# Optimization experiments

Hardware: AMD Instinct MI355X
Metric: run time of the kernel (lower is better)

## Reference

```python
import jax, jax.numpy as jnp
import numpy as np

N_NODES = 50000
N_EDGES = 800000
N_FEATS = 64
K_HOPS = 3


def setup_inputs() -> dict:
    key = jax.random.key(0)
    k1, k2, k3 = jax.random.split(key, 3)
    x = jax.random.normal(k1, (N_NODES, N_FEATS), dtype=jnp.float32)
    edge_index = jax.random.randint(k2, (2, N_EDGES), 0, N_NODES, dtype=jnp.int32)
    # SGConv linear: out_channels = 1 (hardcoded in Net)
    W = jax.random.normal(k3, (1, N_FEATS), dtype=jnp.float32) / np.sqrt(N_FEATS)
    b = jnp.zeros((1,), dtype=jnp.float32)
    return {"x": x, "edge_index": edge_index, "W": W, "b": b}


def reference(x, edge_index, W, b):
    # SGConv: X' = (D^-1/2 (A + I) D^-1/2)^K X @ W.T + b
    N = x.shape[0]
    self_loops = jnp.arange(N, dtype=edge_index.dtype)
    row = jnp.concatenate([edge_index[0], self_loops])  # source nodes (x_j)
    col = jnp.concatenate([edge_index[1], self_loops])  # destination nodes
    # gcn_norm: degree computed at destination with unit edge weights
    deg = jax.ops.segment_sum(jnp.ones(row.shape[0], x.dtype), col, num_segments=N)
    dinv = jnp.where(deg > 0, jax.lax.rsqrt(deg), jnp.zeros_like(deg))
    norm = dinv[row] * dinv[col]  # [E + N]
    # K hops of normalized sparse propagation: out[col] += norm * x[row]
    for _ in range(K_HOPS):
        x = jax.ops.segment_sum(norm[:, None] * x[row], col, num_segments=N)
    return x @ W.T + b  # [N, 1]
```

## Files before the change

kernel.cpp:

```cpp
#include <hip/hip_runtime.h>
#include <hip/hip_bf16.h>

#define N_NODES 50000
#define N_EDGES 800000
#define N_FEATS 64
#define EB4     (N_EDGES / 4)
#define NBUCK   256
#define BRANGE  196
#define CAPB    4096
#define BZT     1024
#define HOPT    1024


__global__ void __launch_bounds__(BZT) k_bucketize(
    const int* __restrict__ row, const int* __restrict__ col,
    int* __restrict__ gcur, unsigned* __restrict__ recs)
{
    __shared__ int s_cnt[NBUCK];
    __shared__ int s_base[NBUCK];
    const int t = threadIdx.x;
    if (t < NBUCK) s_cnt[t] = 0;
    __syncthreads();

    const int g = blockIdx.x * BZT + t;
    const bool valid = g < EB4;
    int4 c4, r4;
    int bk[4], rk[4];
    if (valid) {
        c4 = ((const int4*)col)[g];
        r4 = ((const int4*)row)[g];
        bk[0] = c4.x / BRANGE; rk[0] = atomicAdd(&s_cnt[bk[0]], 1);
        bk[1] = c4.y / BRANGE; rk[1] = atomicAdd(&s_cnt[bk[1]], 1);
        bk[2] = c4.z / BRANGE; rk[2] = atomicAdd(&s_cnt[bk[2]], 1);
        bk[3] = c4.w / BRANGE; rk[3] = atomicAdd(&s_cnt[bk[3]], 1);
    }
    __syncthreads();
    if (t < NBUCK) {
        int n = s_cnt[t];
        s_base[t] = n ? atomicAdd(&gcur[t], n) : 0;
    }
    __syncthreads();
    if (valid) {
        int cc[4] = {c4.x, c4.y, c4.z, c4.w};
        int rr[4] = {r4.x, r4.y, r4.z, r4.w};
        #pragma unroll
        for (int i = 0; i < 4; i++) {
            int slot = s_base[bk[i]] + rk[i];
            unsigned rec = ((unsigned)(cc[i] - bk[i] * BRANGE) << 16) | (unsigned)rr[i];
            if (slot < CAPB) recs[(size_t)bk[i] * CAPB + slot] = rec;
        }
    }
}

__global__ void __launch_bounds__(512) k_prep(
    const int* __restrict__ gcur, const unsigned* __restrict__ recs,
    const float* __restrict__ x, const float* __restrict__ w,
    float* __restrict__ dinv, float* __restrict__ z0)
{
    __shared__ int   s_cnt[BRANGE];
    __shared__ float s_dinv[BRANGE];
    const int t = threadIdx.x;
    const int blk = blockIdx.x;
    const int own0 = blk * BRANGE;
    if (t < BRANGE) s_cnt[t] = 0;
    __syncthreads();

    const int sz  = min(gcur[blk], CAPB);
    const int sz2 = sz >> 1;
    const uint2* rb2 = (const uint2*)(recs + (size_t)blk * CAPB);
    for (int e = t; e < sz2; e += 512) {
        uint2 r = rb2[e];
        atomicAdd(&s_cnt[r.x >> 16], 1);
        atomicAdd(&s_cnt[r.y >> 16], 1);
    }
    if (t == 0 && (sz & 1)) {
        unsigned r = recs[(size_t)blk * CAPB + sz - 1];
        atomicAdd(&s_cnt[r >> 16], 1);
    }
    __syncthreads();

    if (t < BRANGE) {
        float d = rsqrtf((float)(s_cnt[t] + 1));
        s_dinv[t] = d;
        int node = own0 + t;
        if (node < N_NODES) dinv[node] = d;
    }
    __syncthreads();

    if (t < BRANGE) {
        int node = own0 + t;
        if (node < N_NODES) {
            const float4* xr = (const float4*)(x + (size_t)node * N_FEATS);
            const float4* wr = (const float4*)w;
            float acc = 0.0f;
            #pragma unroll
            for (int k = 0; k < N_FEATS / 4; k++) {
                float4 v = xr[k];
                float4 u = wr[k];
                acc += v.x * u.x + v.y * u.y + v.z * u.z + v.w * u.w;
            }
            z0[node] = s_dinv[t] * acc;
        }
    }
}

template <bool FINAL>
__global__ void __launch_bounds__(HOPT) k_hop(
    const int* __restrict__ gcur, const unsigned* __restrict__ recs,
    const float* __restrict__ dinv, const float* __restrict__ zin,
    float* __restrict__ out, const float* __restrict__ bptr)
{
    __shared__ float acc[BRANGE];
    const int t = threadIdx.x;
    const int blk = blockIdx.x;
    if (t < BRANGE) acc[t] = 0.0f;
    __syncthreads();
    const int sz  = min(gcur[blk], CAPB);
    const int sz2 = sz >> 1;
    const uint2* rb2 = (const uint2*)(recs + (size_t)blk * CAPB);
    for (int e = t; e < sz2; e += HOPT) {
        uint2 r = rb2[e];
        atomicAdd(&acc[r.x >> 16], zin[r.x & 0xFFFFu]);
        atomicAdd(&acc[r.y >> 16], zin[r.y & 0xFFFFu]);
    }
    if (t == 0 && (sz & 1)) {
        unsigned r = recs[(size_t)blk * CAPB + sz - 1];
        atomicAdd(&acc[r >> 16], zin[r & 0xFFFFu]);
    }
    __syncthreads();
    if (t < BRANGE) {
        int node = blk * BRANGE + t;
        if (node < N_NODES) {
            float d = dinv[node];
            float v = zin[node] + acc[t];
            out[node] = FINAL ? (d * v + bptr[0]) : (d * d * v);
        }
    }
}


extern "C" void kernel_launch(void* const* d_in, const int* in_sizes, int n_in,
                              void* d_out, int out_size, void* d_ws, size_t ws_size,
                              hipStream_t stream) {
    const float* x  = (const float*)d_in[0];
    const int*   ei = (const int*)d_in[1];
    const float* W  = (const float*)d_in[2];
    const float* b  = (const float*)d_in[3];
    float* out = (float*)d_out;

    const int* row = ei;
    const int* col = ei + N_EDGES;

    int*      gcur = (int*)d_ws;
    unsigned* recs = (unsigned*)(gcur + NBUCK);
    float*    dinv = (float*)(recs + (size_t)NBUCK * CAPB);
    float*    z0   = dinv + N_NODES;
    float*    z1   = z0 + N_NODES;

    hipMemsetAsync(gcur, 0, NBUCK * sizeof(int), stream);

    k_bucketize<<<(EB4 + BZT - 1) / BZT, BZT, 0, stream>>>(row, col, gcur, recs);
    k_prep<<<NBUCK, 512, 0, stream>>>(gcur, recs, x, W, dinv, z0);

    k_hop<false><<<NBUCK, HOPT, 0, stream>>>(gcur, recs, dinv, z0, z1, nullptr);
    k_hop<false><<<NBUCK, HOPT, 0, stream>>>(gcur, recs, dinv, z1, z0, nullptr);
    k_hop<true ><<<NBUCK, HOPT, 0, stream>>>(gcur, recs, dinv, z0, out, b);
}
```

Measured before the change: 102.0 us.

## Stage bucketized edge records in LDS for coalesced writes; widen prep and hop loads

The bucketize kernel now computes a block-local prefix sum over bucket counts and stages records in shared memory sorted by bucket, then writes them out contiguously, so global stores to each bucket become coalesced rather than scattered. The prep kernel moves to 1024 threads and splits each node's 64-feature dot product across 4 lanes, reduced with shuffles. The hop kernel reads four records per uint4 load and issues all four gathers before the LDS atomics. The trade-off is 32KB of extra shared memory per bucketize block, which may limit occupancy, plus extra barriers.

```diff
diff --git a/kernel.cpp b/kernel.cpp
--- a/kernel.cpp
+++ b/kernel.cpp
@@ -17,7 +17,13 @@
     int* __restrict__ gcur, unsigned* __restrict__ recs)
 {
     __shared__ int s_cnt[NBUCK];
-    __shared__ int s_base[NBUCK];
+    __shared__ int s_off[NBUCK];
+    __shared__ int s_gbase[NBUCK];
+    __shared__ int s_wsum[4];
+    __shared__ int s_total;
+    __shared__ unsigned s_buf[BZT * 4];
+    __shared__ unsigned s_adr[BZT * 4];
+
     const int t = threadIdx.x;
     if (t < NBUCK) s_cnt[t] = 0;
     __syncthreads();
@@ -35,24 +41,54 @@
         bk[3] = c4.w / BRANGE; rk[3] = atomicAdd(&s_cnt[bk[3]], 1);
     }
     __syncthreads();
+
     if (t < NBUCK) {
-        int n = s_cnt[t];
-        s_base[t] = n ? atomicAdd(&gcur[t], n) : 0;
-    }
-    __syncthreads();
+        const int lane = t & 63;
+        const int cnt = s_cnt[t];
+        int val = cnt;
+        #pragma unroll
+        for (int d = 1; d < 64; d <<= 1) {
+            int tmp = __shfl_up(val, d);
+            if (lane >= d) val += tmp;
+        }
+        if (lane == 63) s_wsum[t >> 6] = val;
+        s_off[t] = val - cnt;
+    }
+    __syncthreads();
+    if (t < NBUCK) {
+        const int w = t >> 6;
+        int base = 0;
+        #pragma unroll
+        for (int i = 0; i < 3; i++) if (i < w) base += s_wsum[i];
+        s_off[t] += base;
+        const int cnt = s_cnt[t];
+        s_gbase[t] = cnt ? atomicAdd(&gcur[t], cnt) : 0;
+        if (t == 0) s_total = s_wsum[0] + s_wsum[1] + s_wsum[2] + s_wsum[3];
+    }
+    __syncthreads();
+
     if (valid) {
         int cc[4] = {c4.x, c4.y, c4.z, c4.w};
         int rr[4] = {r4.x, r4.y, r4.z, r4.w};
         #pragma unroll
         for (int i = 0; i < 4; i++) {
-            int slot = s_base[bk[i]] + rk[i];
-            unsigned rec = ((unsigned)(cc[i] - bk[i] * BRANGE) << 16) | (unsigned)rr[i];
-            if (slot < CAPB) recs[(size_t)bk[i] * CAPB + slot] = rec;
-        }
-    }
-}
-
-__global__ void __launch_bounds__(512) k_prep(
+            const int b = bk[i];
+            const int p = s_off[b] + rk[i];
+            const int slot = s_gbase[b] + rk[i];
+            s_buf[p] = ((unsigned)(cc[i] - b * BRANGE) << 16) | (unsigned)rr[i];
+            s_adr[p] = (slot < CAPB) ? (unsigned)(b * CAPB + slot) : 0xFFFFFFFFu;
+        }
+    }
+    __syncthreads();
+
+    const int total = s_total;
+    for (int p = t; p < total; p += BZT) {
+        const unsigned a = s_adr[p];
+        if (a != 0xFFFFFFFFu) recs[a] = s_buf[p];
+    }
+}
+
+__global__ void __launch_bounds__(1024) k_prep(
     const int* __restrict__ gcur, const unsigned* __restrict__ recs,
     const float* __restrict__ x, const float* __restrict__ w,
     float* __restrict__ dinv, float* __restrict__ z0)
@@ -68,7 +104,7 @@
     const int sz  = min(gcur[blk], CAPB);
     const int sz2 = sz >> 1;
     const uint2* rb2 = (const uint2*)(recs + (size_t)blk * CAPB);
-    for (int e = t; e < sz2; e += 512) {
+    for (int e = t; e < sz2; e += 1024) {
         uint2 r = rb2[e];
         atomicAdd(&s_cnt[r.x >> 16], 1);
         atomicAdd(&s_cnt[r.y >> 16], 1);
@@ -87,19 +123,23 @@
     }
     __syncthreads();
 
-    if (t < BRANGE) {
-        int node = own0 + t;
+    const int ln = t >> 2;
+    const int pp = t & 3;
+    if (ln < BRANGE) {
+        int node = own0 + ln;
         if (node < N_NODES) {
-            const float4* xr = (const float4*)(x + (size_t)node * N_FEATS);
-            const float4* wr = (const float4*)w;
+            const float4* xr = (const float4*)(x + (size_t)node * N_FEATS + pp * 16);
+            const float4* wr = (const float4*)(w + pp * 16);
             float acc = 0.0f;
             #pragma unroll
-            for (int k = 0; k < N_FEATS / 4; k++) {
+            for (int k = 0; k < 4; k++) {
                 float4 v = xr[k];
                 float4 u = wr[k];
                 acc += v.x * u.x + v.y * u.y + v.z * u.z + v.w * u.w;
             }
-            z0[node] = s_dinv[t] * acc;
+            acc += __shfl_xor(acc, 1);
+            acc += __shfl_xor(acc, 2);
+            if (pp == 0) z0[node] = s_dinv[ln] * acc;
         }
     }
 }
@@ -116,15 +156,21 @@
     if (t < BRANGE) acc[t] = 0.0f;
     __syncthreads();
     const int sz  = min(gcur[blk], CAPB);
-    const int sz2 = sz >> 1;
-    const uint2* rb2 = (const uint2*)(recs + (size_t)blk * CAPB);
-    for (int e = t; e < sz2; e += HOPT) {
-        uint2 r = rb2[e];
-        atomicAdd(&acc[r.x >> 16], zin[r.x & 0xFFFFu]);
-        atomicAdd(&acc[r.y >> 16], zin[r.y & 0xFFFFu]);
-    }
-    if (t == 0 && (sz & 1)) {
-        unsigned r = recs[(size_t)blk * CAPB + sz - 1];
+    const int sz4 = sz >> 2;
+    const uint4* rb4 = (const uint4*)(recs + (size_t)blk * CAPB);
+    for (int e = t; e < sz4; e += HOPT) {
+        uint4 r = rb4[e];
+        float v0 = zin[r.x & 0xFFFFu];
+        float v1 = zin[r.y & 0xFFFFu];
+        float v2 = zin[r.z & 0xFFFFu];
+        float v3 = zin[r.w & 0xFFFFu];
+        atomicAdd(&acc[r.x >> 16], v0);
+        atomicAdd(&acc[r.y >> 16], v1);
+        atomicAdd(&acc[r.z >> 16], v2);
+        atomicAdd(&acc[r.w >> 16], v3);
+    }
+    if (t < (sz & 3)) {
+        unsigned r = recs[(size_t)blk * CAPB + (sz4 << 2) + t];
         atomicAdd(&acc[r >> 16], zin[r & 0xFFFFu]);
     }
     __syncthreads();
@@ -160,7 +206,7 @@
     hipMemsetAsync(gcur, 0, NBUCK * sizeof(int), stream);
 
     k_bucketize<<<(EB4 + BZT - 1) / BZT, BZT, 0, stream>>>(row, col, gcur, recs);
-    k_prep<<<NBUCK, 512, 0, stream>>>(gcur, recs, x, W, dinv, z0);
+    k_prep<<<NBUCK, 1024, 0, stream>>>(gcur, recs, x, W, dinv, z0);
 
     k_hop<false><<<NBUCK, HOPT, 0, stream>>>(gcur, recs, dinv, z0, z1, nullptr);
     k_hop<false><<<NBUCK, HOPT, 0, stream>>>(gcur, recs, dinv, z1, z0, nullptr);
```

New measurement: 98.84 us. -3.1%, faster.
